# Kernel optimization log

Measured on AMD Instinct MI355X. Metric: run time of the kernel, lower is better.

## Reference

```python
import jax, jax.numpy as jnp
import numpy as np

X_DIM = 40
N_BATCH = 65536


def _circ_conv1d(x, W, b, pad):
    # x: [N, C_in, L], W: [C_out, C_in, K] (torch layout), circular padding
    if pad > 0:
        x = jnp.pad(x, ((0, 0), (0, 0), (pad, pad)), mode='wrap')
    y = jax.lax.conv_general_dilated(x, W, window_strides=(1,), padding='VALID',
                                     dimension_numbers=('NCH', 'OIH', 'NCH'))
    return y + b[None, :, None]


def setup_inputs() -> dict:
    key = jax.random.key(0)
    ks = jax.random.split(key, 9)
    u = jax.random.normal(ks[0], (N_BATCH, X_DIM), dtype=jnp.float32)
    coeff = jax.random.normal(ks[1], (18,), dtype=jnp.float32) * 0.1
    # Conv1d params, torch layout [out_ch, in_ch, kernel], kaiming-ish scale
    W1 = jax.random.normal(ks[2], (72, 1, 5), dtype=jnp.float32) * (1.0 / np.sqrt(1 * 5))
    b1 = jax.random.normal(ks[3], (72,), dtype=jnp.float32) * 0.05
    W2 = jax.random.normal(ks[4], (37, 48, 5), dtype=jnp.float32) * (1.0 / np.sqrt(48 * 5))
    b2 = jax.random.normal(ks[5], (37,), dtype=jnp.float32) * 0.05
    W3 = jax.random.normal(ks[6], (1, 37, 1), dtype=jnp.float32) * (1.0 / np.sqrt(37))
    b3 = jax.random.normal(ks[7], (1,), dtype=jnp.float32) * 0.05
    t = jnp.zeros((1,), dtype=jnp.float32)  # unused by the module, kept for signature fidelity
    return {"t": t, "u": u, "coeff": coeff, "W1": W1, "b1": b1,
            "W2": W2, "b2": b2, "W3": W3, "b3": b3}


def reference(t, u, coeff, W1, b1, W2, b2, W3, b3):
    # circular neighbor gathers: index_select with (i+k)%D == roll by -k
    u_m2 = jnp.roll(u, 2, axis=-1)
    u_m1 = jnp.roll(u, 1, axis=-1)
    u_p1 = jnp.roll(u, -1, axis=-1)
    u_p2 = jnp.roll(u, -2, axis=-1)
    feats = jnp.stack([
        jnp.ones_like(u),
        u_m2, u_m1, u, u_p1, u_p2,
        u_m2 ** 2, u_m1 ** 2, u ** 2, u_p1 ** 2, u_p2 ** 2,
        u_m2 * u_m1, u_m1 * u, u * u_p1, u_p1 * u_p2,
        u_m2 * u, u_m1 * u_p1, u * u_p2,
    ], axis=-1)  # [N, D, 18]
    out1 = feats @ coeff  # [N, D]

    x = u[:, None, :]  # [N, 1, D]
    h = jax.nn.relu(_circ_conv1d(x, W1, b1, 2))  # [N, 72, D]
    h = jnp.concatenate([h[:, :24], h[:, 24:48] * h[:, 48:]], axis=1)  # [N, 48, D]
    h = jax.nn.relu(_circ_conv1d(h, W2, b2, 2))  # [N, 37, D]
    out2 = _circ_conv1d(h, W3, b3, 0)[:, 0, :]  # [N, D]
    return out1 + out2
```

## Files before the change

kernel.cpp:

```cpp
#include <hip/hip_runtime.h>
#include <hip/hip_bf16.h>

typedef short s16x8 __attribute__((ext_vector_type(8)));
typedef short s16x4 __attribute__((ext_vector_type(4)));
typedef float f32x4 __attribute__((ext_vector_type(4)));

#define TB 8
#define NBG 8
#define HALO 46
#define GSTRIDE 2216
#define USTRIDE 50
#define NT 3
#define GT_SHORTS (TB * GSTRIDE)

__device__ __forceinline__ unsigned short f2bf(float f) {
    unsigned int u = __float_as_uint(f);
    u += 0x7fff + ((u >> 16) & 1);
    return (unsigned short)(u >> 16);
}

__device__ __forceinline__ unsigned int pk_bf16(float lo, float hi) {
    float2 f; f.x = lo; f.y = hi;
    __hip_bfloat162 h = __float22bfloat162_rn(f);
    union { __hip_bfloat162 b; unsigned int u; } c;
    c.b = h;
    return c.u;
}

__global__ __launch_bounds__(256, 2) void lorenz96_fused(
    const float* __restrict__ u,
    const float* __restrict__ coeff,
    const float* __restrict__ W1,
    const float* __restrict__ b1,
    const float* __restrict__ W2,
    const float* __restrict__ b2,
    const float* __restrict__ W3,
    const float* __restrict__ b3,
    float* __restrict__ out)
{
    __shared__ __align__(16) unsigned short gtile[2][GT_SHORTS];
    __shared__ __align__(16) float u_sbuf[2][TB * USTRIDE];
    __shared__ float out1_sb[2][TB * 40];

    unsigned short* B_lds = &gtile[0][0];

    const int t    = threadIdx.x;
    const int lane = t & 63;
    const int wave = t >> 6;
    const int quad = lane >> 4;
    const int l15  = lane & 15;

    const int b0_block = blockIdx.x * (TB * NBG);

    for (int g = t; g < NT * 8 * 64; g += 256) {
        int lg = g & 63;
        int ks = (g >> 6) & 7;
        int nt = g >> 9;
        int o  = nt * 16 + (lg & 15);
        int kb = ks * 32 + (lg >> 4) * 8;
        s16x8 pack = {0, 0, 0, 0, 0, 0, 0, 0};
        #pragma unroll
        for (int j = 0; j < 8; ++j) {
            int k = kb + j;
            if (o < 37) {
                if (k < 240) {
                    int c = k % 48, tap = k / 48;
                    pack[j] = (short)f2bf(W2[o * 240 + c * 5 + tap]);
                } else if (k == 240) {
                    pack[j] = (short)f2bf(b2[o]);
                }
            }
        }
        *(s16x8*)&B_lds[g * 8] = pack;
    }

    s16x8 aW1[5];
    {
        int chs[5];
        chs[0] = l15; chs[1] = 16 + l15; chs[2] = 32 + l15;
        chs[3] = (l15 >= 8) ? 40 + l15 : -1;
        chs[4] = 56 + l15;
        #pragma unroll
        for (int mt = 0; mt < 5; ++mt) {
            s16x8 a = {0, 0, 0, 0, 0, 0, 0, 0};
            int ch = chs[mt];
            if (quad == 0 && ch >= 0) {
                #pragma unroll
                for (int j = 0; j < 5; ++j) a[j] = (short)f2bf(W1[ch * 5 + j]);
                a[5] = (short)f2bf(b1[ch]);
            }
            aW1[mt] = a;
        }
    }

    float w3v[NT][4];
    #pragma unroll
    for (int nt = 0; nt < NT; ++nt)
        #pragma unroll
        for (int r = 0; r < 4; ++r) {
            int o = nt * 16 + quad * 4 + r;
            w3v[nt][r] = (o < 37) ? W3[o] : 0.f;
        }
    const float b3v = b3[0];
    float cf[18];
    #pragma unroll
    for (int i = 0; i < 18; ++i) cf[i] = coeff[i];

    auto prestage_u = [&](int grp) {
        for (int idx = t; idx < TB * USTRIDE; idx += 256) {
            int b = idx / USTRIDE, k = idx - b * USTRIDE;
            int gi = k + 36; gi -= (gi >= 40) ? 40 : 0; gi -= (gi >= 40) ? 40 : 0;
            u_sbuf[grp & 1][idx] = u[(size_t)(b0_block + grp * TB + b) * 40 + gi];
        }
    };

    auto poly = [&](int grp) {
        const float* u_s = u_sbuf[grp & 1];
        float* o1 = out1_sb[grp & 1];
        #pragma unroll
        for (int pass = 0; pass < 2; ++pass) {
            int i = pass ? 4 : quad;
            bool act = pass ? (quad == 0) : true;
            if (act) {
                int m = (wave + 4 * i) * 16 + l15;
                int p = m >> 3, b = m & 7;
                const float* us = &u_s[b * USTRIDE + p];
                float um2 = us[2], um1 = us[3], u0 = us[4], up1 = us[5], up2 = us[6];
                float r = cf[0] + cf[1]*um2 + cf[2]*um1 + cf[3]*u0 + cf[4]*up1 + cf[5]*up2
                        + cf[6]*um2*um2 + cf[7]*um1*um1 + cf[8]*u0*u0 + cf[9]*up1*up1 + cf[10]*up2*up2
                        + cf[11]*um2*um1 + cf[12]*um1*u0 + cf[13]*u0*up1 + cf[14]*up1*up2
                        + cf[15]*um2*u0 + cf[16]*um1*up1 + cf[17]*u0*up2;
                o1[m] = r;
            }
        }
    };

    auto phase2 = [&](int grp) {
        const float* u_s = u_sbuf[grp & 1];
        unsigned short* gt = &gtile[grp & 1][0];
        #pragma unroll
        for (int i = 0; i < 6; ++i) {
            const int ct  = wave + 4 * i;
            const int col = ct * 16 + l15;
            const int b = col & 7, h = col >> 3;
            const int hc = (h < HALO) ? h : 0;
            s16x8 bU = {0, 0, 0, 0, 0, 0, 0, 0};
            if (quad == 0) {
                const float* us = &u_s[b * USTRIDE + hc];
                union { s16x8 v; unsigned int w[4]; } bu;
                bu.w[0] = pk_bf16(us[0], us[1]);
                bu.w[1] = pk_bf16(us[2], us[3]);
                bu.w[2] = pk_bf16(us[4], 1.0f);
                bu.w[3] = 0;
                bU = bu.v;
            }
            f32x4 a0 = {0.f,0.f,0.f,0.f}, a1 = a0, a2 = a0, a3 = a0, a4 = a0;
            a0 = __builtin_amdgcn_mfma_f32_16x16x32_bf16(aW1[0], bU, a0, 0, 0, 0);
            a1 = __builtin_amdgcn_mfma_f32_16x16x32_bf16(aW1[1], bU, a1, 0, 0, 0);
            a2 = __builtin_amdgcn_mfma_f32_16x16x32_bf16(aW1[2], bU, a2, 0, 0, 0);
            a3 = __builtin_amdgcn_mfma_f32_16x16x32_bf16(aW1[3], bU, a3, 0, 0, 0);
            a4 = __builtin_amdgcn_mfma_f32_16x16x32_bf16(aW1[4], bU, a4, 0, 0, 0);
            if (h < HALO) {
                float v0[4], v1[4], v2[4];
                #pragma unroll
                for (int r = 0; r < 4; ++r) {
                    v0[r] = fmaxf(a0[r], 0.f);
                    v1[r] = fmaxf(a1[r], 0.f);
                    if (quad >= 2) v1[r] *= fmaxf(a3[r], 0.f);
                    v2[r] = fmaxf(a2[r], 0.f) * fmaxf(a4[r], 0.f);
                }
                union { s16x4 v; unsigned int w[2]; } w0, w1, w2;
                w0.w[0] = pk_bf16(v0[0], v0[1]); w0.w[1] = pk_bf16(v0[2], v0[3]);
                w1.w[0] = pk_bf16(v1[0], v1[1]); w1.w[1] = pk_bf16(v1[2], v1[3]);
                w2.w[0] = pk_bf16(v2[0], v2[1]); w2.w[1] = pk_bf16(v2[2], v2[3]);
                unsigned short* gp = &gt[b * GSTRIDE + h * 48 + quad * 4];
                *(s16x4*)(gp)      = w0.v;
                *(s16x4*)(gp + 16) = w1.v;
                *(s16x4*)(gp + 32) = w2.v;
            }
        }
    };

    prestage_u(0);
    __syncthreads();

    s16x8 aW2[NT][8];
    #pragma unroll
    for (int nt = 0; nt < NT; ++nt)
        #pragma unroll
        for (int ks = 0; ks < 8; ++ks)
            aW2[nt][ks] = *(const s16x8*)&B_lds[((nt * 8 + ks) * 64 + lane) * 8];

    poly(0);
    prestage_u(1);
    __syncthreads();

    phase2(0);
    __syncthreads();

    for (int g = 0; g < NBG; ++g) {
        const int b0 = b0_block + g * TB;
        const unsigned short* gt = &gtile[g & 1][0];
        const float* o1 = out1_sb[g & 1];

        #pragma unroll
        for (int i = 0; i < 5; ++i) {
            const int mt = wave + 4 * i;
            const int m  = mt * 16 + l15;
            const int p  = m >> 3, b = m & 7;
            const unsigned short* gbase = &gt[b * GSTRIDE + p * 48 + quad * 8];
            s16x8 bg[8];
            #pragma unroll
            for (int ks = 0; ks < 8; ++ks) bg[ks] = *(const s16x8*)(gbase + ks * 32);
            {
                s16x8 b7 = bg[7];
                if (quad == 2) b7[0] = (short)0x3F80;
                bg[7] = b7;
            }
            f32x4 c0 = {0.f,0.f,0.f,0.f}, c1 = c0, c2 = c0;
            #pragma unroll
            for (int ks = 0; ks < 8; ++ks) {
                c0 = __builtin_amdgcn_mfma_f32_16x16x32_bf16(aW2[0][ks], bg[ks], c0, 0, 0, 0);
                c1 = __builtin_amdgcn_mfma_f32_16x16x32_bf16(aW2[1][ks], bg[ks], c1, 0, 0, 0);
                c2 = __builtin_amdgcn_mfma_f32_16x16x32_bf16(aW2[2][ks], bg[ks], c2, 0, 0, 0);
            }
            float s = 0.f;
            #pragma unroll
            for (int r = 0; r < 4; ++r) {
                s += fmaxf(c0[r], 0.f) * w3v[0][r];
                s += fmaxf(c1[r], 0.f) * w3v[1][r];
                s += fmaxf(c2[r], 0.f) * w3v[2][r];
            }
            s += __shfl_xor(s, 16, 64);
            s += __shfl_xor(s, 32, 64);
            if (lane < 16) {
                int mo = mt * 16 + lane;
                out[(size_t)(b0 + (mo & 7)) * 40 + (mo >> 3)] = s + b3v + o1[mo];
            }
        }

        if (g + 1 < NBG) {
            poly(g + 1);
            phase2(g + 1);
            if (g + 2 < NBG) prestage_u(g + 2);
            __syncthreads();
        }
    }
}

extern "C" void kernel_launch(void* const* d_in, const int* in_sizes, int n_in,
                              void* d_out, int out_size, void* d_ws, size_t ws_size,
                              hipStream_t stream) {
    const float* u     = (const float*)d_in[1];
    const float* coeff = (const float*)d_in[2];
    const float* W1    = (const float*)d_in[3];
    const float* b1    = (const float*)d_in[4];
    const float* W2    = (const float*)d_in[5];
    const float* b2    = (const float*)d_in[6];
    const float* W3    = (const float*)d_in[7];
    const float* b3    = (const float*)d_in[8];
    float* out = (float*)d_out;

    const int n_batch = in_sizes[1] / 40;
    const int grid = n_batch / (TB * NBG);
    lorenz96_fused<<<grid, 256, 0, stream>>>(u, coeff, W1, b1, W2, b2, W3, b3, out);
}
```

Baseline: 194.2 us.

## Single-buffer gtile and raise occupancy to three blocks per CU

Drops the double-buffered gtile and out1 staging in shared memory so LDS per block roughly halves, and raises launch bounds from 2 to 3 blocks per CU. Halves the batch groups per block, so more blocks are launched. Splits the conv2 B-operand loads into two halves of four to cut live registers. The cost is that the phase2 producer no longer overlaps the MFMA consumer inside a block, and an extra barrier is added per group. The design relies on the extra resident blocks to hide that latency instead.

```diff
diff --git a/kernel.cpp b/kernel.cpp
--- a/kernel.cpp
+++ b/kernel.cpp
@@ -6,7 +6,7 @@
 typedef float f32x4 __attribute__((ext_vector_type(4)));
 
 #define TB 8
-#define NBG 8
+#define NBG 4
 #define HALO 46
 #define GSTRIDE 2216
 #define USTRIDE 50
@@ -27,7 +27,7 @@
     return c.u;
 }
 
-__global__ __launch_bounds__(256, 2) void lorenz96_fused(
+__global__ __launch_bounds__(256, 3) void lorenz96_fused(
     const float* __restrict__ u,
     const float* __restrict__ coeff,
     const float* __restrict__ W1,
@@ -38,11 +38,11 @@
     const float* __restrict__ b3,
     float* __restrict__ out)
 {
-    __shared__ __align__(16) unsigned short gtile[2][GT_SHORTS];
+    __shared__ __align__(16) unsigned short gtile[GT_SHORTS];
     __shared__ __align__(16) float u_sbuf[2][TB * USTRIDE];
-    __shared__ float out1_sb[2][TB * 40];
-
-    unsigned short* B_lds = &gtile[0][0];
+    __shared__ float out1_s[TB * 40];
+
+    unsigned short* B_lds = gtile;
 
     const int t    = threadIdx.x;
     const int lane = t & 63;
@@ -116,7 +116,6 @@
 
     auto poly = [&](int grp) {
         const float* u_s = u_sbuf[grp & 1];
-        float* o1 = out1_sb[grp & 1];
         #pragma unroll
         for (int pass = 0; pass < 2; ++pass) {
             int i = pass ? 4 : quad;
@@ -130,14 +129,13 @@
                         + cf[6]*um2*um2 + cf[7]*um1*um1 + cf[8]*u0*u0 + cf[9]*up1*up1 + cf[10]*up2*up2
                         + cf[11]*um2*um1 + cf[12]*um1*u0 + cf[13]*u0*up1 + cf[14]*up1*up2
                         + cf[15]*um2*u0 + cf[16]*um1*up1 + cf[17]*u0*up2;
-                o1[m] = r;
+                out1_s[m] = r;
             }
         }
     };
 
     auto phase2 = [&](int grp) {
         const float* u_s = u_sbuf[grp & 1];
-        unsigned short* gt = &gtile[grp & 1][0];
         #pragma unroll
         for (int i = 0; i < 6; ++i) {
             const int ct  = wave + 4 * i;
@@ -173,7 +171,7 @@
                 w0.w[0] = pk_bf16(v0[0], v0[1]); w0.w[1] = pk_bf16(v0[2], v0[3]);
                 w1.w[0] = pk_bf16(v1[0], v1[1]); w1.w[1] = pk_bf16(v1[2], v1[3]);
                 w2.w[0] = pk_bf16(v2[0], v2[1]); w2.w[1] = pk_bf16(v2[2], v2[3]);
-                unsigned short* gp = &gt[b * GSTRIDE + h * 48 + quad * 4];
+                unsigned short* gp = &gtile[b * GSTRIDE + h * 48 + quad * 4];
                 *(s16x4*)(gp)      = w0.v;
                 *(s16x4*)(gp + 16) = w1.v;
                 *(s16x4*)(gp + 32) = w2.v;
@@ -191,38 +189,46 @@
         for (int ks = 0; ks < 8; ++ks)
             aW2[nt][ks] = *(const s16x8*)&B_lds[((nt * 8 + ks) * 64 + lane) * 8];
 
-    poly(0);
-    prestage_u(1);
-    __syncthreads();
-
-    phase2(0);
-    __syncthreads();
-
     for (int g = 0; g < NBG; ++g) {
         const int b0 = b0_block + g * TB;
-        const unsigned short* gt = &gtile[g & 1][0];
-        const float* o1 = out1_sb[g & 1];
+
+        __syncthreads();
+
+        poly(g);
+        phase2(g);
+        if (g + 1 < NBG) prestage_u(g + 1);
+
+        __syncthreads();
 
         #pragma unroll
         for (int i = 0; i < 5; ++i) {
             const int mt = wave + 4 * i;
             const int m  = mt * 16 + l15;
             const int p  = m >> 3, b = m & 7;
-            const unsigned short* gbase = &gt[b * GSTRIDE + p * 48 + quad * 8];
-            s16x8 bg[8];
-            #pragma unroll
-            for (int ks = 0; ks < 8; ++ks) bg[ks] = *(const s16x8*)(gbase + ks * 32);
+            const unsigned short* gbase = &gtile[b * GSTRIDE + p * 48 + quad * 8];
+            f32x4 c0 = {0.f,0.f,0.f,0.f}, c1 = c0, c2 = c0;
             {
-                s16x8 b7 = bg[7];
-                if (quad == 2) b7[0] = (short)0x3F80;
-                bg[7] = b7;
-            }
-            f32x4 c0 = {0.f,0.f,0.f,0.f}, c1 = c0, c2 = c0;
-            #pragma unroll
-            for (int ks = 0; ks < 8; ++ks) {
-                c0 = __builtin_amdgcn_mfma_f32_16x16x32_bf16(aW2[0][ks], bg[ks], c0, 0, 0, 0);
-                c1 = __builtin_amdgcn_mfma_f32_16x16x32_bf16(aW2[1][ks], bg[ks], c1, 0, 0, 0);
-                c2 = __builtin_amdgcn_mfma_f32_16x16x32_bf16(aW2[2][ks], bg[ks], c2, 0, 0, 0);
+                s16x8 bg[4];
+                #pragma unroll
+                for (int ks = 0; ks < 4; ++ks) bg[ks] = *(const s16x8*)(gbase + ks * 32);
+                #pragma unroll
+                for (int ks = 0; ks < 4; ++ks) {
+                    c0 = __builtin_amdgcn_mfma_f32_16x16x32_bf16(aW2[0][ks], bg[ks], c0, 0, 0, 0);
+                    c1 = __builtin_amdgcn_mfma_f32_16x16x32_bf16(aW2[1][ks], bg[ks], c1, 0, 0, 0);
+                    c2 = __builtin_amdgcn_mfma_f32_16x16x32_bf16(aW2[2][ks], bg[ks], c2, 0, 0, 0);
+                }
+            }
+            {
+                s16x8 bg[4];
+                #pragma unroll
+                for (int ks = 0; ks < 4; ++ks) bg[ks] = *(const s16x8*)(gbase + (4 + ks) * 32);
+                if (quad == 2) { s16x8 b7 = bg[3]; b7[0] = (short)0x3F80; bg[3] = b7; }
+                #pragma unroll
+                for (int ks = 0; ks < 4; ++ks) {
+                    c0 = __builtin_amdgcn_mfma_f32_16x16x32_bf16(aW2[0][4 + ks], bg[ks], c0, 0, 0, 0);
+                    c1 = __builtin_amdgcn_mfma_f32_16x16x32_bf16(aW2[1][4 + ks], bg[ks], c1, 0, 0, 0);
+                    c2 = __builtin_amdgcn_mfma_f32_16x16x32_bf16(aW2[2][4 + ks], bg[ks], c2, 0, 0, 0);
+                }
             }
             float s = 0.f;
             #pragma unroll
@@ -235,15 +241,8 @@
             s += __shfl_xor(s, 32, 64);
             if (lane < 16) {
                 int mo = mt * 16 + lane;
-                out[(size_t)(b0 + (mo & 7)) * 40 + (mo >> 3)] = s + b3v + o1[mo];
-            }
-        }
-
-        if (g + 1 < NBG) {
-            poly(g + 1);
-            phase2(g + 1);
-            if (g + 2 < NBG) prestage_u(g + 2);
-            __syncthreads();
+                out[(size_t)(b0 + (mo & 7)) * 40 + (mo >> 3)] = s + b3v + out1_s[mo];
+            }
         }
     }
 }
```

Result: slower. 226.8 us (+16.8%).

## Interleave conv2 and next-group conv1 tiles, double groups per block

Applied to the files above, without the earlier changes.

Restructures the per-group loop so each iteration interleaves the conv2/output tiles of the current group with the conv1 MFMA tiles of the next group, and issues the global prestage of u earlier in the iteration. The aim is to let MFMA work from both stages overlap and to hide LDS and global latency. It also doubles groups per block, which halves the grid and amortises weight loads, and pads the gtile stride, likely to change LDS bank mapping. In phase2, out-of-range halo columns now write to a dummy padded row instead of branching, at the cost of extra LDS and fewer blocks in flight.

```diff
diff --git a/kernel.cpp b/kernel.cpp
--- a/kernel.cpp
+++ b/kernel.cpp
@@ -6,9 +6,9 @@
 typedef float f32x4 __attribute__((ext_vector_type(4)));
 
 #define TB 8
-#define NBG 8
+#define NBG 16
 #define HALO 46
-#define GSTRIDE 2216
+#define GSTRIDE 2264
 #define USTRIDE 50
 #define NT 3
 #define GT_SHORTS (TB * GSTRIDE)
@@ -106,6 +106,8 @@
     #pragma unroll
     for (int i = 0; i < 18; ++i) cf[i] = coeff[i];
 
+    s16x8 aW2[NT][8];
+
     auto prestage_u = [&](int grp) {
         for (int idx = t; idx < TB * USTRIDE; idx += 256) {
             int b = idx / USTRIDE, k = idx - b * USTRIDE;
@@ -135,56 +137,82 @@
         }
     };
 
-    auto phase2 = [&](int grp) {
-        const float* u_s = u_sbuf[grp & 1];
-        unsigned short* gt = &gtile[grp & 1][0];
-        #pragma unroll
-        for (int i = 0; i < 6; ++i) {
-            const int ct  = wave + 4 * i;
-            const int col = ct * 16 + l15;
-            const int b = col & 7, h = col >> 3;
-            const int hc = (h < HALO) ? h : 0;
-            s16x8 bU = {0, 0, 0, 0, 0, 0, 0, 0};
-            if (quad == 0) {
-                const float* us = &u_s[b * USTRIDE + hc];
-                union { s16x8 v; unsigned int w[4]; } bu;
-                bu.w[0] = pk_bf16(us[0], us[1]);
-                bu.w[1] = pk_bf16(us[2], us[3]);
-                bu.w[2] = pk_bf16(us[4], 1.0f);
-                bu.w[3] = 0;
-                bU = bu.v;
-            }
-            f32x4 a0 = {0.f,0.f,0.f,0.f}, a1 = a0, a2 = a0, a3 = a0, a4 = a0;
-            a0 = __builtin_amdgcn_mfma_f32_16x16x32_bf16(aW1[0], bU, a0, 0, 0, 0);
-            a1 = __builtin_amdgcn_mfma_f32_16x16x32_bf16(aW1[1], bU, a1, 0, 0, 0);
-            a2 = __builtin_amdgcn_mfma_f32_16x16x32_bf16(aW1[2], bU, a2, 0, 0, 0);
-            a3 = __builtin_amdgcn_mfma_f32_16x16x32_bf16(aW1[3], bU, a3, 0, 0, 0);
-            a4 = __builtin_amdgcn_mfma_f32_16x16x32_bf16(aW1[4], bU, a4, 0, 0, 0);
-            if (h < HALO) {
-                float v0[4], v1[4], v2[4];
-                #pragma unroll
-                for (int r = 0; r < 4; ++r) {
-                    v0[r] = fmaxf(a0[r], 0.f);
-                    v1[r] = fmaxf(a1[r], 0.f);
-                    if (quad >= 2) v1[r] *= fmaxf(a3[r], 0.f);
-                    v2[r] = fmaxf(a2[r], 0.f) * fmaxf(a4[r], 0.f);
-                }
-                union { s16x4 v; unsigned int w[2]; } w0, w1, w2;
-                w0.w[0] = pk_bf16(v0[0], v0[1]); w0.w[1] = pk_bf16(v0[2], v0[3]);
-                w1.w[0] = pk_bf16(v1[0], v1[1]); w1.w[1] = pk_bf16(v1[2], v1[3]);
-                w2.w[0] = pk_bf16(v2[0], v2[1]); w2.w[1] = pk_bf16(v2[2], v2[3]);
-                unsigned short* gp = &gt[b * GSTRIDE + h * 48 + quad * 4];
-                *(s16x4*)(gp)      = w0.v;
-                *(s16x4*)(gp + 16) = w1.v;
-                *(s16x4*)(gp + 32) = w2.v;
-            }
+    auto p2_tile = [&](int i, const float* u_s, unsigned short* gt) {
+        const int ct  = wave + 4 * i;
+        const int col = ct * 16 + l15;
+        const int b = col & 7, h = col >> 3;
+        const int hc = (h < HALO) ? h : 0;
+        const int hs = (h < HALO) ? h : HALO;
+        const float* us = &u_s[b * USTRIDE + hc];
+        float t0 = us[0], t1 = us[1], t2 = us[2], t3 = us[3], t4 = us[4];
+        const bool q0 = (quad == 0);
+        union { s16x8 v; unsigned int w[4]; } bu;
+        bu.w[0] = q0 ? pk_bf16(t0, t1) : 0u;
+        bu.w[1] = q0 ? pk_bf16(t2, t3) : 0u;
+        bu.w[2] = q0 ? pk_bf16(t4, 1.0f) : 0u;
+        bu.w[3] = 0u;
+        f32x4 a0 = {0.f,0.f,0.f,0.f}, a1 = a0, a2 = a0, a3 = a0, a4 = a0;
+        a0 = __builtin_amdgcn_mfma_f32_16x16x32_bf16(aW1[0], bu.v, a0, 0, 0, 0);
+        a1 = __builtin_amdgcn_mfma_f32_16x16x32_bf16(aW1[1], bu.v, a1, 0, 0, 0);
+        a2 = __builtin_amdgcn_mfma_f32_16x16x32_bf16(aW1[2], bu.v, a2, 0, 0, 0);
+        a3 = __builtin_amdgcn_mfma_f32_16x16x32_bf16(aW1[3], bu.v, a3, 0, 0, 0);
+        a4 = __builtin_amdgcn_mfma_f32_16x16x32_bf16(aW1[4], bu.v, a4, 0, 0, 0);
+        float v0[4], v1[4], v2[4];
+        #pragma unroll
+        for (int r = 0; r < 4; ++r) {
+            v0[r] = fmaxf(a0[r], 0.f);
+            v1[r] = fmaxf(a1[r], 0.f);
+            if (quad >= 2) v1[r] *= fmaxf(a3[r], 0.f);
+            v2[r] = fmaxf(a2[r], 0.f) * fmaxf(a4[r], 0.f);
+        }
+        union { s16x4 v; unsigned int w[2]; } w0, w1, w2;
+        w0.w[0] = pk_bf16(v0[0], v0[1]); w0.w[1] = pk_bf16(v0[2], v0[3]);
+        w1.w[0] = pk_bf16(v1[0], v1[1]); w1.w[1] = pk_bf16(v1[2], v1[3]);
+        w2.w[0] = pk_bf16(v2[0], v2[1]); w2.w[1] = pk_bf16(v2[2], v2[3]);
+        unsigned short* gp = &gt[b * GSTRIDE + hs * 48 + quad * 4];
+        *(s16x4*)(gp)      = w0.v;
+        *(s16x4*)(gp + 16) = w1.v;
+        *(s16x4*)(gp + 32) = w2.v;
+    };
+
+    auto p3_tile = [&](int i, const unsigned short* gt, const float* o1, int b0) {
+        const int mt = wave + 4 * i;
+        const int m  = mt * 16 + l15;
+        const int p  = m >> 3, b = m & 7;
+        const unsigned short* gbase = &gt[b * GSTRIDE + p * 48 + quad * 8];
+        s16x8 bg[8];
+        #pragma unroll
+        for (int ks = 0; ks < 8; ++ks) bg[ks] = *(const s16x8*)(gbase + ks * 32);
+        {
+            s16x8 b7 = bg[7];
+            if (quad == 2) b7[0] = (short)0x3F80;
+            bg[7] = b7;
+        }
+        f32x4 c0 = {0.f,0.f,0.f,0.f}, c1 = c0, c2 = c0;
+        #pragma unroll
+        for (int ks = 0; ks < 8; ++ks) {
+            c0 = __builtin_amdgcn_mfma_f32_16x16x32_bf16(aW2[0][ks], bg[ks], c0, 0, 0, 0);
+            c1 = __builtin_amdgcn_mfma_f32_16x16x32_bf16(aW2[1][ks], bg[ks], c1, 0, 0, 0);
+            c2 = __builtin_amdgcn_mfma_f32_16x16x32_bf16(aW2[2][ks], bg[ks], c2, 0, 0, 0);
+        }
+        float s = 0.f;
+        #pragma unroll
+        for (int r = 0; r < 4; ++r) {
+            s += fmaxf(c0[r], 0.f) * w3v[0][r];
+            s += fmaxf(c1[r], 0.f) * w3v[1][r];
+            s += fmaxf(c2[r], 0.f) * w3v[2][r];
+        }
+        s += __shfl_xor(s, 16, 64);
+        s += __shfl_xor(s, 32, 64);
+        if (lane < 16) {
+            int mo = mt * 16 + lane;
+            out[(size_t)(b0 + (mo & 7)) * 40 + (mo >> 3)] = s + b3v + o1[mo];
         }
     };
 
     prestage_u(0);
     __syncthreads();
 
-    s16x8 aW2[NT][8];
     #pragma unroll
     for (int nt = 0; nt < NT; ++nt)
         #pragma unroll
@@ -195,56 +223,34 @@
     prestage_u(1);
     __syncthreads();
 
-    phase2(0);
+    #pragma unroll
+    for (int i = 0; i < 6; ++i) p2_tile(i, u_sbuf[0], &gtile[0][0]);
     __syncthreads();
 
-    for (int g = 0; g < NBG; ++g) {
+    for (int g = 0; g < NBG - 1; ++g) {
         const int b0 = b0_block + g * TB;
-        const unsigned short* gt = &gtile[g & 1][0];
-        const float* o1 = out1_sb[g & 1];
-
-        #pragma unroll
-        for (int i = 0; i < 5; ++i) {
-            const int mt = wave + 4 * i;
-            const int m  = mt * 16 + l15;
-            const int p  = m >> 3, b = m & 7;
-            const unsigned short* gbase = &gt[b * GSTRIDE + p * 48 + quad * 8];
-            s16x8 bg[8];
-            #pragma unroll
-            for (int ks = 0; ks < 8; ++ks) bg[ks] = *(const s16x8*)(gbase + ks * 32);
-            {
-                s16x8 b7 = bg[7];
-                if (quad == 2) b7[0] = (short)0x3F80;
-                bg[7] = b7;
-            }
-            f32x4 c0 = {0.f,0.f,0.f,0.f}, c1 = c0, c2 = c0;
-            #pragma unroll
-            for (int ks = 0; ks < 8; ++ks) {
-                c0 = __builtin_amdgcn_mfma_f32_16x16x32_bf16(aW2[0][ks], bg[ks], c0, 0, 0, 0);
-                c1 = __builtin_amdgcn_mfma_f32_16x16x32_bf16(aW2[1][ks], bg[ks], c1, 0, 0, 0);
-                c2 = __builtin_amdgcn_mfma_f32_16x16x32_bf16(aW2[2][ks], bg[ks], c2, 0, 0, 0);
-            }
-            float s = 0.f;
-            #pragma unroll
-            for (int r = 0; r < 4; ++r) {
-                s += fmaxf(c0[r], 0.f) * w3v[0][r];
-                s += fmaxf(c1[r], 0.f) * w3v[1][r];
-                s += fmaxf(c2[r], 0.f) * w3v[2][r];
-            }
-            s += __shfl_xor(s, 16, 64);
-            s += __shfl_xor(s, 32, 64);
-            if (lane < 16) {
-                int mo = mt * 16 + lane;
-                out[(size_t)(b0 + (mo & 7)) * 40 + (mo >> 3)] = s + b3v + o1[mo];
-            }
-        }
-
-        if (g + 1 < NBG) {
-            poly(g + 1);
-            phase2(g + 1);
-            if (g + 2 < NBG) prestage_u(g + 2);
-            __syncthreads();
-        }
+        const unsigned short* gt   = &gtile[g & 1][0];
+        unsigned short*       gtn  = &gtile[(g + 1) & 1][0];
+        const float*          o1   = out1_sb[g & 1];
+        const float*          u_n  = u_sbuf[(g + 1) & 1];
+
+        if (g + 2 < NBG) prestage_u(g + 2);
+
+        #pragma unroll
+        for (int i = 0; i < 6; ++i) {
+            if (i < 5) p3_tile(i, gt, o1, b0);
+            p2_tile(i, u_n, gtn);
+        }
+
+        poly(g + 1);
+        __syncthreads();
+    }
+
+    {
+        const int g = NBG - 1;
+        const int b0 = b0_block + g * TB;
+        #pragma unroll
+        for (int i = 0; i < 5; ++i) p3_tile(i, &gtile[g & 1][0], out1_sb[g & 1], b0);
     }
 }
 
```

Result: faster. 186.8 us (-3.8%).
